# Optimization experiments

Hardware: AMD Instinct MI355X
Metric: run time of the kernel (lower is better)

## Reference

```python
import jax, jax.numpy as jnp
import numpy as np

N_NODES = 100000
N_EDGES = 1600000
IN_F, HID, OUT_F = 50, 256, 121


def setup_inputs() -> dict:
    key = jax.random.key(0)
    ks = jax.random.split(key, 8)
    x = jax.random.normal(ks[0], (N_NODES, IN_F), dtype=jnp.float32)
    edge_index = jax.random.randint(ks[1], (2, N_EDGES), 0, N_NODES, dtype=jnp.int64)
    W1 = jax.random.normal(ks[2], (IN_F, HID), dtype=jnp.float32) * (1.0 / np.sqrt(IN_F))
    b1 = jnp.zeros((HID,), dtype=jnp.float32)
    W2 = jax.random.normal(ks[3], (HID, HID), dtype=jnp.float32) * (1.0 / np.sqrt(HID))
    b2 = jnp.zeros((HID,), dtype=jnp.float32)
    W3 = jax.random.normal(ks[4], (HID, OUT_F), dtype=jnp.float32) * (1.0 / np.sqrt(HID))
    b3 = jnp.zeros((OUT_F,), dtype=jnp.float32)
    return {"x": x, "edge_index": edge_index, "W1": W1, "b1": b1,
            "W2": W2, "b2": b2, "W3": W3, "b3": b3}


def _gcn_norm(edge_index, num_nodes):
    # PyG gcn_norm: add self-loops, symmetric degree normalization.
    loop = jnp.arange(num_nodes, dtype=edge_index.dtype)
    row = jnp.concatenate([edge_index[0], loop])  # source
    col = jnp.concatenate([edge_index[1], loop])  # target (aggregation dim)
    ones = jnp.ones(row.shape[0], dtype=jnp.float32)
    deg = jax.ops.segment_sum(ones, col, num_segments=num_nodes)
    dinv = jnp.where(deg > 0, jax.lax.rsqrt(deg), 0.0)
    norm = dinv[row] * dinv[col]  # [E+N]
    return row, col, norm


def _gcn_conv(x, W, b, row, col, norm, num_nodes):
    h = x @ W                                   # [N, F_out] dense transform
    msg = h[row] * norm[:, None]                # gather + scale  [E+N, F_out]
    agg = jax.ops.segment_sum(msg, col, num_segments=num_nodes)  # scatter-add
    return agg + b


def reference(x, edge_index, W1, b1, W2, b2, W3, b3):
    n = x.shape[0]
    row, col, norm = _gcn_norm(edge_index, n)
    # layer 1 + relu (dropout is identity in eval mode)
    x1 = _gcn_conv(x, W1, b1, row, col, norm, n)
    h = jax.nn.relu(x1)
    # layer 2 + relu
    x1 = _gcn_conv(h, W2, b2, row, col, norm, n)
    h = jax.nn.relu(x1)
    # layer 3; module returns pre-relu output x1 of the last conv
    x1 = _gcn_conv(h, W3, b3, row, col, norm, n)
    return x1
```

## Files before the change

kernel.cpp:

```cpp
#include <hip/hip_runtime.h>


#define IN_F 50
#define HID  256
#define OUT_F 121
#define KP1  64
#define NP3  128
#define MPAD 100096

typedef __attribute__((ext_vector_type(8))) short bf16x8;
typedef __attribute__((ext_vector_type(4))) float f32x4;

__device__ __forceinline__ float bf2f(unsigned short u) {
    union { unsigned int i; float f; } x; x.i = ((unsigned int)u) << 16; return x.f;
}
__device__ __forceinline__ unsigned short f2bf(float f) {
    union { float f; unsigned int i; } x; x.f = f;
    unsigned int r = x.i + 0x7FFFu + ((x.i >> 16) & 1u);
    return (unsigned short)(r >> 16);
}

__device__ __forceinline__ void gl2lds16(const void* g, void* l) {
    __builtin_amdgcn_global_load_lds(
        (const __attribute__((address_space(1))) void*)g,
        (__attribute__((address_space(3))) void*)l, 16, 0, 0);
}

__global__ void k_detect(const int* __restrict__ ei, int* __restrict__ flag, int N) {
    int i = threadIdx.x;
    int lo = ei[2 * i], hi = ei[2 * i + 1];
    int bad = (hi != 0) || ((unsigned)lo >= (unsigned)N);
    unsigned long long m = __ballot(bad);
    if (threadIdx.x == 0) *flag = (m == 0ULL) ? 1 : 0;
}


__global__ void k_count(const int* __restrict__ ei, const int* __restrict__ flag,
                        int* __restrict__ cnt, int E, int N) {
    int t = blockIdx.x * blockDim.x + threadIdx.x;
    if (t >= E) return;
    int f = *flag;
    int c = f ? ei[2 * (E + t)] : ei[E + t];
    c = min(max(c, 0), N - 1);
    atomicAdd(&cnt[c], 1);
}

__global__ __launch_bounds__(1024) void k_scan(const int* __restrict__ cnt,
                                               int* __restrict__ offs,
                                               float* __restrict__ dinv, int n) {
    __shared__ int wsum[16];
    __shared__ int s_carry;
    int lane = threadIdx.x & 63, wid = threadIdx.x >> 6;
    if (threadIdx.x == 0) s_carry = 0;
    __syncthreads();
    for (int base = 0; base < n; base += 4096) {
        int i0 = base + (int)threadIdx.x * 4;
        int v0 = (i0 + 0 < n) ? cnt[i0 + 0] : 0;
        int v1 = (i0 + 1 < n) ? cnt[i0 + 1] : 0;
        int v2 = (i0 + 2 < n) ? cnt[i0 + 2] : 0;
        int v3 = (i0 + 3 < n) ? cnt[i0 + 3] : 0;
        int s1 = v0 + v1, s2 = s1 + v2, tsum = s2 + v3;
        int x = tsum;
        #pragma unroll
        for (int d = 1; d < 64; d <<= 1) {
            int y = __shfl_up(x, d, 64);
            if (lane >= d) x += y;
        }
        if (lane == 63) wsum[wid] = x;
        __syncthreads();
        int wpre = 0;
        #pragma unroll
        for (int j = 0; j < 16; j++) wpre += (j < wid) ? wsum[j] : 0;
        int carry = s_carry;
        int e0 = carry + wpre + x - tsum;
        if (i0 + 0 < n) { offs[i0+0]=e0;    dinv[i0+0]=rsqrtf((float)(v0+1)); }
        if (i0 + 1 < n) { offs[i0+1]=e0+v0; dinv[i0+1]=rsqrtf((float)(v1+1)); }
        if (i0 + 2 < n) { offs[i0+2]=e0+s1; dinv[i0+2]=rsqrtf((float)(v2+1)); }
        if (i0 + 3 < n) { offs[i0+3]=e0+s2; dinv[i0+3]=rsqrtf((float)(v3+1)); }
        __syncthreads();
        if (threadIdx.x == 1023) s_carry = carry + wpre + x;
        __syncthreads();
    }
    if (threadIdx.x == 0) offs[n] = s_carry;
}

__global__ void k_fill8(const int* __restrict__ ei, const int* __restrict__ flag,
                        const int* __restrict__ offs,
                        int* __restrict__ fillc, int* __restrict__ rowidx,
                        int E, int N, int rng) {
    int cell = blockIdx.x & 7;
    int t = (blockIdx.x >> 3) * blockDim.x + threadIdx.x;
    if (t >= E) return;
    int f = *flag;
    int c = f ? ei[2 * (E + t)] : ei[E + t];
    c = min(max(c, 0), N - 1);
    int lo = cell * rng;
    int hi = min(lo + rng, N);
    if (c < lo || c >= hi) return;
    int r = f ? ei[2 * t] : ei[t];
    r = min(max(r, 0), N - 1);
    int pos = offs[c] + atomicAdd(&fillc[c], 1);
    if ((unsigned)pos < (unsigned)E) rowidx[pos] = r;
}

__global__ void k_prep(const float* __restrict__ x, const float* __restrict__ dinv,
                       unsigned short* __restrict__ Xs,
                       const float* __restrict__ W1, unsigned short* __restrict__ Bt1,
                       const float* __restrict__ W2, unsigned short* __restrict__ Bt2,
                       const float* __restrict__ W3, unsigned short* __restrict__ Bt3,
                       int N) {
    int bid = blockIdx.x;
    int npadx = (N * KP1 + 255) / 256;
    if (bid < npadx) {
        int idx = bid * 256 + (int)threadIdx.x;
        if (idx < N * KP1) {
            int node = idx >> 6, k = idx & 63;
            Xs[idx] = (k < IN_F) ? f2bf(dinv[node] * x[node * IN_F + k]) : (unsigned short)0;
        }
        return;
    }
    bid -= npadx;
    if (bid < (HID * KP1) / 256) {
        int idx = bid * 256 + (int)threadIdx.x;
        int nn = idx >> 6, k = idx & 63;
        Bt1[idx] = (k < IN_F) ? f2bf(W1[k * HID + nn]) : (unsigned short)0;
        return;
    }
    bid -= (HID * KP1) / 256;
    if (bid < (HID * HID) / 256) {
        int idx = bid * 256 + (int)threadIdx.x;
        int nn = idx >> 8, k = idx & 255;
        Bt2[idx] = f2bf(W2[k * HID + nn]);
        return;
    }
    bid -= (HID * HID) / 256;
    {
        int idx = bid * 256 + (int)threadIdx.x;
        int nn = idx >> 8, k = idx & 255;
        Bt3[idx] = (nn < OUT_F) ? f2bf(W3[k * OUT_F + nn]) : (unsigned short)0;
    }
}

__global__ __launch_bounds__(256) void k_gemm_lds(const unsigned short* __restrict__ A,
                                                  const unsigned short* __restrict__ Bt,
                                                  const float* __restrict__ dinv,
                                                  const float* __restrict__ bias,
                                                  unsigned short* __restrict__ C,
                                                  int K, int Nout,
                                                  int BIAS, int RELU, int SCALE) {
    __shared__ char lds[16384];
    const int tid = threadIdx.x;
    const int wid = tid >> 6, lane = tid & 63;
    const int wm = wid & 1, wn = wid >> 1;
    const int quad = lane >> 4, ml = lane & 15;
    const int m0 = blockIdx.x * 128;
    const int n0g = blockIdx.y * 128;

    f32x4 acc[4][4];
    #pragma unroll
    for (int a = 0; a < 4; a++)
        #pragma unroll
        for (int b = 0; b < 4; b++) acc[a][b] = (f32x4){0.f, 0.f, 0.f, 0.f};

    for (int kk = 0; kk < K; kk += 32) {
        #pragma unroll
        for (int r = 0; r < 2; r++) {
            int c = r * 256 + tid;
            int row = c >> 2, q = c & 3;
            gl2lds16(A  + (size_t)(m0  + row) * K + kk + q * 8, lds + c * 16);
            gl2lds16(Bt + (size_t)(n0g + row) * K + kk + q * 8, lds + 8192 + c * 16);
        }
        __syncthreads();
        bf16x8 af[4], bfv[4];
        #pragma unroll
        for (int mf = 0; mf < 4; mf++)
            af[mf] = *(const bf16x8*)(lds + ((wm * 64 + mf * 16 + ml) * 64 + quad * 16));
        #pragma unroll
        for (int nf = 0; nf < 4; nf++)
            bfv[nf] = *(const bf16x8*)(lds + 8192 + ((wn * 64 + nf * 16 + ml) * 64 + quad * 16));
        #pragma unroll
        for (int mf = 0; mf < 4; mf++)
            #pragma unroll
            for (int nf = 0; nf < 4; nf++)
                acc[mf][nf] = __builtin_amdgcn_mfma_f32_16x16x32_bf16(af[mf], bfv[nf], acc[mf][nf], 0, 0, 0);
        __syncthreads();
    }

    #pragma unroll
    for (int mf = 0; mf < 4; mf++) {
        int r0 = m0 + wm * 64 + mf * 16 + quad * 4;
        float dd[4] = {1.f, 1.f, 1.f, 1.f};
        if (SCALE) { dd[0]=dinv[r0]; dd[1]=dinv[r0+1]; dd[2]=dinv[r0+2]; dd[3]=dinv[r0+3]; }
        #pragma unroll
        for (int nf = 0; nf < 4; nf++) {
            int col = n0g + wn * 64 + nf * 16 + ml;
            float bb = BIAS ? bias[col] : 0.f;
            #pragma unroll
            for (int i = 0; i < 4; i++) {
                float v = acc[mf][nf][i] + bb;
                if (RELU) v = fmaxf(v, 0.f);
                v *= dd[i];
                C[(size_t)(r0 + i) * Nout + col] = f2bf(v);
            }
        }
    }
}

__global__ __launch_bounds__(256) void k_mlp23(const unsigned short* __restrict__ A,
                                               const unsigned short* __restrict__ B2t,
                                               const unsigned short* __restrict__ B3t,
                                               const float* __restrict__ b2,
                                               const float* __restrict__ dinv,
                                               unsigned short* __restrict__ G) {
    __shared__ char lds[65536];
    const int tid = threadIdx.x;
    const int wid = tid >> 6, lane = tid & 63;
    const int wm = wid & 1, wn = wid >> 1;
    const int quad = lane >> 4, ml = lane & 15;
    const int m0 = blockIdx.x * 128;

    f32x4 acc1[4][8];
    #pragma unroll
    for (int a = 0; a < 4; a++)
        #pragma unroll
        for (int b = 0; b < 8; b++) acc1[a][b] = (f32x4){0.f, 0.f, 0.f, 0.f};

    for (int kk = 0; kk < HID; kk += 32) {
        #pragma unroll
        for (int r = 0; r < 2; r++) {
            int c = r * 256 + tid;
            int row = c >> 2, q = c & 3;
            gl2lds16(A + (size_t)(m0 + row) * HID + kk + q * 8, lds + c * 16);
        }
        #pragma unroll
        for (int r = 0; r < 4; r++) {
            int c = r * 256 + tid;
            int nn = c >> 2, q = c & 3;
            gl2lds16(B2t + (size_t)nn * HID + kk + q * 8, lds + 8192 + c * 16);
        }
        __syncthreads();
        bf16x8 af[4], bv[8];
        #pragma unroll
        for (int mf = 0; mf < 4; mf++)
            af[mf] = *(const bf16x8*)(lds + ((wm * 64 + mf * 16 + ml) * 64 + quad * 16));
        #pragma unroll
        for (int nf = 0; nf < 8; nf++)
            bv[nf] = *(const bf16x8*)(lds + 8192 + ((wn * 128 + nf * 16 + ml) * 64 + quad * 16));
        #pragma unroll
        for (int mf = 0; mf < 4; mf++)
            #pragma unroll
            for (int nf = 0; nf < 8; nf++)
                acc1[mf][nf] = __builtin_amdgcn_mfma_f32_16x16x32_bf16(af[mf], bv[nf], acc1[mf][nf], 0, 0, 0);
        __syncthreads();
    }

    #pragma unroll
    for (int nf = 0; nf < 8; nf++) {
        int col = wn * 128 + nf * 16 + ml;
        float bb = b2[col];
        #pragma unroll
        for (int mf = 0; mf < 4; mf++) {
            int rl = wm * 64 + mf * 16 + quad * 4;
            #pragma unroll
            for (int i = 0; i < 4; i++) {
                int row = rl + i;
                int byte = (row * 512 + col * 2) ^ ((row & 7) << 4);
                *(unsigned short*)(lds + byte) = f2bf(fmaxf(acc1[mf][nf][i] + bb, 0.f));
            }
        }
    }
    __syncthreads();

    f32x4 acc2[4][4];
    #pragma unroll
    for (int a = 0; a < 4; a++)
        #pragma unroll
        for (int b = 0; b < 4; b++) acc2[a][b] = (f32x4){0.f, 0.f, 0.f, 0.f};

    for (int kk = 0; kk < HID; kk += 32) {
        bf16x8 af2[4], bv2[4];
        #pragma unroll
        for (int mf = 0; mf < 4; mf++) {
            int row = wm * 64 + mf * 16 + ml;
            int byte = (row * 512 + kk * 2 + quad * 16) ^ ((row & 7) << 4);
            af2[mf] = *(const bf16x8*)(lds + byte);
        }
        #pragma unroll
        for (int nf = 0; nf < 4; nf++)
            bv2[nf] = *(const bf16x8*)(B3t + (size_t)(wn * 64 + nf * 16 + ml) * HID + kk + quad * 8);
        #pragma unroll
        for (int mf = 0; mf < 4; mf++)
            #pragma unroll
            for (int nf = 0; nf < 4; nf++)
                acc2[mf][nf] = __builtin_amdgcn_mfma_f32_16x16x32_bf16(af2[mf], bv2[nf], acc2[mf][nf], 0, 0, 0);
    }

    #pragma unroll
    for (int mf = 0; mf < 4; mf++) {
        int r0 = m0 + wm * 64 + mf * 16 + quad * 4;
        float dd[4] = {dinv[r0], dinv[r0+1], dinv[r0+2], dinv[r0+3]};
        #pragma unroll
        for (int nf = 0; nf < 4; nf++) {
            int col = wn * 64 + nf * 16 + ml;
            #pragma unroll
            for (int i = 0; i < 4; i++)
                G[(size_t)(r0 + i) * NP3 + col] = f2bf(acc2[mf][nf][i] * dd[i]);
        }
    }
}


__device__ __forceinline__ int rclamp(int r, int N) { return min(max(r, 0), N - 1); }

__global__ void k_aggx(const unsigned short* __restrict__ Xs,
                       const int* __restrict__ offs, const int* __restrict__ rowidx,
                       const float* __restrict__ dinv, unsigned short* __restrict__ Y, int N) {
    int wid = threadIdx.x >> 6, lane = threadIdx.x & 63;
    int sub = lane >> 3, sl = lane & 7;
    int node = blockIdx.x * 32 + wid * 8 + sub;
    int nc = min(node, N - 1);
    int c = sl * 8;
    bf16x8 s = *(const bf16x8*)(Xs + (size_t)nc * KP1 + c);
    float a[8];
    #pragma unroll
    for (int k = 0; k < 8; k++) a[k] = bf2f((unsigned short)s[k]);
    int e = offs[nc], end = offs[nc + 1];
    if (node >= N) { e = 0; end = 0; }
    while (__any(e < end)) {
        int r[4]; float m[4];
        #pragma unroll
        for (int j = 0; j < 4; j++) {
            int idx = e + j;
            m[j] = (idx < end) ? 1.f : 0.f;
            idx = min(idx, end - 1); idx = max(idx, 0);
            r[j] = rclamp(rowidx[idx], N);
        }
        bf16x8 u[4];
        #pragma unroll
        for (int j = 0; j < 4; j++)
            u[j] = *(const bf16x8*)(Xs + (size_t)r[j] * KP1 + c);
        #pragma unroll
        for (int j = 0; j < 4; j++)
            #pragma unroll
            for (int k = 0; k < 8; k++)
                a[k] = fmaf(bf2f((unsigned short)u[j][k]), m[j], a[k]);
        e += 4;
    }
    if (node < N) {
        float dv = dinv[node];
        bf16x8 o;
        #pragma unroll
        for (int k = 0; k < 8; k++) o[k] = (short)f2bf(a[k] * dv);
        *(bf16x8*)(Y + (size_t)node * KP1 + c) = o;
    }
}

__global__ void k_agg256s(const unsigned short* __restrict__ Hn,
                          const int* __restrict__ offs, const int* __restrict__ rowidx,
                          const float* __restrict__ dinv, unsigned short* __restrict__ Y,
                          int N, int half_n) {
    int cell = blockIdx.x & 7;
    int chunk = cell >> 1, half = cell & 1;
    int idx = blockIdx.x >> 3;
    int wid = threadIdx.x >> 6, lane = threadIdx.x & 63;
    int sub = lane >> 3, sl = lane & 7;
    int node = half * half_n + idx * 32 + wid * 8 + sub;
    int hi_end = min((half + 1) * half_n, N);
    int ok = node < hi_end;
    int nc = ok ? node : hi_end - 1;
    int c = chunk * 64 + sl * 8;
    bf16x8 s = *(const bf16x8*)(Hn + (size_t)nc * HID + c);
    float a[8];
    #pragma unroll
    for (int k = 0; k < 8; k++) a[k] = bf2f((unsigned short)s[k]);
    int e = offs[nc], end = offs[nc + 1];
    if (!ok) { e = 0; end = 0; }
    while (__any(e < end)) {
        int r[4]; float m[4];
        #pragma unroll
        for (int j = 0; j < 4; j++) {
            int idx2 = e + j;
            m[j] = (idx2 < end) ? 1.f : 0.f;
            idx2 = min(idx2, end - 1); idx2 = max(idx2, 0);
            r[j] = rclamp(rowidx[idx2], N);
        }
        bf16x8 u[4];
        #pragma unroll
        for (int j = 0; j < 4; j++)
            u[j] = *(const bf16x8*)(Hn + (size_t)r[j] * HID + c);
        #pragma unroll
        for (int j = 0; j < 4; j++)
            #pragma unroll
            for (int k = 0; k < 8; k++)
                a[k] = fmaf(bf2f((unsigned short)u[j][k]), m[j], a[k]);
        e += 4;
    }
    if (ok) {
        float dv = dinv[node];
        bf16x8 o;
        #pragma unroll
        for (int k = 0; k < 8; k++) o[k] = (short)f2bf(a[k] * dv);
        *(bf16x8*)(Y + (size_t)node * HID + c) = o;
    }
}

__global__ void k_aggouts(const unsigned short* __restrict__ G,
                          const int* __restrict__ offs, const int* __restrict__ rowidx,
                          const float* __restrict__ dinv, const float* __restrict__ bias,
                          float* __restrict__ out, int N, int quar_n) {
    int cell = blockIdx.x & 7;
    int chunk = cell >> 2, quar = cell & 3;
    int idx = blockIdx.x >> 3;
    int wid = threadIdx.x >> 6, lane = threadIdx.x & 63;
    int sub = lane >> 3, sl = lane & 7;
    int node = quar * quar_n + idx * 32 + wid * 8 + sub;
    int hi_end = min((quar + 1) * quar_n, N);
    int ok = node < hi_end;
    int nc = ok ? node : hi_end - 1;
    int c = chunk * 64 + sl * 8;
    bf16x8 s = *(const bf16x8*)(G + (size_t)nc * NP3 + c);
    float a[8];
    #pragma unroll
    for (int k = 0; k < 8; k++) a[k] = bf2f((unsigned short)s[k]);
    int e = offs[nc], end = offs[nc + 1];
    if (!ok) { e = 0; end = 0; }
    while (__any(e < end)) {
        int r[4]; float m[4];
        #pragma unroll
        for (int j = 0; j < 4; j++) {
            int idx2 = e + j;
            m[j] = (idx2 < end) ? 1.f : 0.f;
            idx2 = min(idx2, end - 1); idx2 = max(idx2, 0);
            r[j] = rclamp(rowidx[idx2], N);
        }
        bf16x8 u[4];
        #pragma unroll
        for (int j = 0; j < 4; j++)
            u[j] = *(const bf16x8*)(G + (size_t)r[j] * NP3 + c);
        #pragma unroll
        for (int j = 0; j < 4; j++)
            #pragma unroll
            for (int k = 0; k < 8; k++)
                a[k] = fmaf(bf2f((unsigned short)u[j][k]), m[j], a[k]);
        e += 4;
    }
    if (ok) {
        float dv = dinv[node];
        #pragma unroll
        for (int k = 0; k < 8; k++) {
            int col = c + k;
            if (col < OUT_F)
                out[(size_t)node * OUT_F + col] = fmaf(a[k], dv, bias[col]);
        }
    }
}


extern "C" void kernel_launch(void* const* d_in, const int* in_sizes, int n_in,
                              void* d_out, int out_size, void* d_ws, size_t ws_size,
                              hipStream_t stream) {
    const float* x  = (const float*)d_in[0];
    const int*   ei = (const int*)d_in[1];
    const float* W1 = (const float*)d_in[2];
    const float* b1 = (const float*)d_in[3];
    const float* W2 = (const float*)d_in[4];
    const float* b2 = (const float*)d_in[5];
    const float* W3 = (const float*)d_in[6];
    const float* b3 = (const float*)d_in[7];
    float* out = (float*)d_out;

    const int N = in_sizes[0] / IN_F;
    const int E = in_sizes[1] / 2;

    char* w = (char*)d_ws;
    size_t off = 0;
    auto alloc = [&](size_t bytes) -> char* {
        char* p = w + off;
        off += (bytes + 255) & ~(size_t)255;
        return p;
    };
    int*   cnt    = (int*)  alloc((size_t)N * 4);
    int*   fillc  = (int*)  alloc((size_t)N * 4);
    int*   offs   = (int*)  alloc((size_t)(N + 1) * 4);
    float* dinv   = (float*)alloc((size_t)MPAD * 4);
    int*   flag   = (int*)  alloc(256);
    int*   rowidx = (int*)  alloc((size_t)E * 4);
    unsigned short* Bt1 = (unsigned short*)alloc((size_t)HID * KP1 * 2);
    unsigned short* Bt2 = (unsigned short*)alloc((size_t)HID * HID * 2);
    unsigned short* Bt3 = (unsigned short*)alloc((size_t)NP3 * HID * 2);
    unsigned short* bufA = (unsigned short*)alloc((size_t)MPAD * HID * 2);
    unsigned short* bufB = (unsigned short*)alloc((size_t)MPAD * HID * 2);
    unsigned short* Xs  = bufA;
    unsigned short* Y1  = bufB;
    unsigned short* H1s = bufA;
    unsigned short* Y2  = bufB;
    unsigned short* G3  = bufA;

    size_t msz = (size_t)((char*)fillc - (char*)cnt) + (size_t)N * 4;
    hipMemsetAsync(cnt, 0, msz, stream);

    k_detect<<<1, 64, 0, stream>>>(ei, flag, N);
    k_count<<<(E + 255) / 256, 256, 0, stream>>>(ei, flag, cnt, E, N);
    k_scan<<<1, 1024, 0, stream>>>(cnt, offs, dinv, N);
    int rng = (N + 7) / 8;
    k_fill8<<<8 * ((E + 255) / 256), 256, 0, stream>>>(ei, flag, offs, fillc, rowidx, E, N, rng);

    int prep_grid = (N * KP1 + 255) / 256 + (HID * KP1) / 256 + (HID * HID) / 256 + (NP3 * HID) / 256;
    k_prep<<<prep_grid, 256, 0, stream>>>(x, dinv, Xs, W1, Bt1, W2, Bt2, W3, Bt3, N);

    k_aggx<<<(N + 31) / 32, 256, 0, stream>>>(Xs, offs, rowidx, dinv, Y1, N);
    dim3 g1(MPAD / 128, HID / 128);
    k_gemm_lds<<<g1, 256, 0, stream>>>(Y1, Bt1, dinv, b1, H1s, KP1, HID, 1, 1, 1);
    int half_n = (N + 1) / 2;
    int bpc2 = (half_n + 31) / 32;
    k_agg256s<<<8 * bpc2, 256, 0, stream>>>(H1s, offs, rowidx, dinv, Y2, N, half_n);
    k_mlp23<<<MPAD / 128, 256, 0, stream>>>(Y2, Bt2, Bt3, b2, dinv, G3);
    int quar_n = (N + 3) / 4;
    int bpc3 = (quar_n + 31) / 32;
    k_aggouts<<<8 * bpc3, 256, 0, stream>>>(G3, offs, rowidx, dinv, b3, out, N, quar_n);

    (void)n_in; (void)out_size; (void)ws_size;
}
```

Measured before the change: 621.6 us.

## Bucket CSR neighbors by source-range quarter and parallelize the offset scan

Builds the CSR with four sub-buckets per target node, keyed by which quarter of the node range the source falls in. Each node's neighbor list is then ordered by source region, so gathers in the aggregation kernels touch more localized memory. The single-block serial scan becomes a three-kernel multi-block scan, and edge indices are converted once to clamped int32 arrays reused by the count and fill passes. The cost is four times larger count and offset arrays, extra kernel launches, and a split inner loop with more wave-divergent tails per node.

Result: faster. 562.8 us (-9.5%).

```diff
diff --git a/kernel.cpp b/kernel.cpp
--- a/kernel.cpp
+++ b/kernel.cpp
@@ -34,72 +34,110 @@
     if (threadIdx.x == 0) *flag = (m == 0ULL) ? 1 : 0;
 }
 
-
-__global__ void k_count(const int* __restrict__ ei, const int* __restrict__ flag,
-                        int* __restrict__ cnt, int E, int N) {
+__global__ void k_cvt(const int* __restrict__ ei, const int* __restrict__ flag,
+                      int* __restrict__ col32, int* __restrict__ row32, int E, int N) {
     int t = blockIdx.x * blockDim.x + threadIdx.x;
     if (t >= E) return;
     int f = *flag;
     int c = f ? ei[2 * (E + t)] : ei[E + t];
-    c = min(max(c, 0), N - 1);
-    atomicAdd(&cnt[c], 1);
-}
-
-__global__ __launch_bounds__(1024) void k_scan(const int* __restrict__ cnt,
-                                               int* __restrict__ offs,
-                                               float* __restrict__ dinv, int n) {
+    int r = f ? ei[2 * t] : ei[t];
+    col32[t] = min(max(c, 0), N - 1);
+    row32[t] = min(max(r, 0), N - 1);
+}
+
+
+__global__ void k_count4(const int* __restrict__ col32, const int* __restrict__ row32,
+                         int* __restrict__ cnt4, int E, int seglen) {
+    int t = blockIdx.x * blockDim.x + threadIdx.x;
+    if (t >= E) return;
+    int c = col32[t], r = row32[t];
+    atomicAdd(&cnt4[c * 4 + r / seglen], 1);
+}
+
+__global__ __launch_bounds__(1024) void k_scanA(const int* __restrict__ cnt4,
+                                                int* __restrict__ bsum, int n) {
+    __shared__ int ws[16];
+    int tid = threadIdx.x, lane = tid & 63, wid = tid >> 6;
+    int j0 = blockIdx.x * 4096 + tid * 4;
+    int t = 0;
+    #pragma unroll
+    for (int j = 0; j < 4; j++) {
+        int node = j0 + j;
+        if (node < n) { int4 v = *(const int4*)(cnt4 + 4 * node); t += v.x + v.y + v.z + v.w; }
+    }
+    #pragma unroll
+    for (int d = 1; d < 64; d <<= 1) t += __shfl_xor(t, d, 64);
+    if (lane == 0) ws[wid] = t;
+    __syncthreads();
+    if (tid == 0) {
+        int s = 0;
+        #pragma unroll
+        for (int j = 0; j < 16; j++) s += ws[j];
+        bsum[blockIdx.x] = s;
+    }
+}
+
+__global__ void k_scanB(const int* __restrict__ bsum, int* __restrict__ bbase,
+                        int* __restrict__ offs4, int nb, int n4) {
+    int lane = threadIdx.x;
+    int v = (lane < nb) ? bsum[lane] : 0;
+    int x = v;
+    #pragma unroll
+    for (int d = 1; d < 64; d <<= 1) { int y = __shfl_up(x, d, 64); if (lane >= d) x += y; }
+    if (lane < nb) bbase[lane] = x - v;
+    if (lane == nb - 1) offs4[n4] = x;
+}
+
+__global__ __launch_bounds__(1024) void k_scanC(const int* __restrict__ cnt4,
+                                                const int* __restrict__ bbase,
+                                                int* __restrict__ offs4,
+                                                float* __restrict__ dinv, int n) {
     __shared__ int wsum[16];
-    __shared__ int s_carry;
-    int lane = threadIdx.x & 63, wid = threadIdx.x >> 6;
-    if (threadIdx.x == 0) s_carry = 0;
+    int tid = threadIdx.x, lane = tid & 63, wid = tid >> 6;
+    int i0 = blockIdx.x * 4096 + tid * 4;
+    int4 z = {0, 0, 0, 0};
+    int4 c0 = (i0 + 0 < n) ? *(const int4*)(cnt4 + 4 * (i0 + 0)) : z;
+    int4 c1 = (i0 + 1 < n) ? *(const int4*)(cnt4 + 4 * (i0 + 1)) : z;
+    int4 c2 = (i0 + 2 < n) ? *(const int4*)(cnt4 + 4 * (i0 + 2)) : z;
+    int4 c3 = (i0 + 3 < n) ? *(const int4*)(cnt4 + 4 * (i0 + 3)) : z;
+    int v0 = c0.x + c0.y + c0.z + c0.w;
+    int v1 = c1.x + c1.y + c1.z + c1.w;
+    int v2 = c2.x + c2.y + c2.z + c2.w;
+    int v3 = c3.x + c3.y + c3.z + c3.w;
+    int s1 = v0 + v1, s2 = s1 + v2, tsum = s2 + v3;
+    int x = tsum;
+    #pragma unroll
+    for (int d = 1; d < 64; d <<= 1) { int y = __shfl_up(x, d, 64); if (lane >= d) x += y; }
+    if (lane == 63) wsum[wid] = x;
     __syncthreads();
-    for (int base = 0; base < n; base += 4096) {
-        int i0 = base + (int)threadIdx.x * 4;
-        int v0 = (i0 + 0 < n) ? cnt[i0 + 0] : 0;
-        int v1 = (i0 + 1 < n) ? cnt[i0 + 1] : 0;
-        int v2 = (i0 + 2 < n) ? cnt[i0 + 2] : 0;
-        int v3 = (i0 + 3 < n) ? cnt[i0 + 3] : 0;
-        int s1 = v0 + v1, s2 = s1 + v2, tsum = s2 + v3;
-        int x = tsum;
-        #pragma unroll
-        for (int d = 1; d < 64; d <<= 1) {
-            int y = __shfl_up(x, d, 64);
-            if (lane >= d) x += y;
-        }
-        if (lane == 63) wsum[wid] = x;
-        __syncthreads();
-        int wpre = 0;
-        #pragma unroll
-        for (int j = 0; j < 16; j++) wpre += (j < wid) ? wsum[j] : 0;
-        int carry = s_carry;
-        int e0 = carry + wpre + x - tsum;
-        if (i0 + 0 < n) { offs[i0+0]=e0;    dinv[i0+0]=rsqrtf((float)(v0+1)); }
-        if (i0 + 1 < n) { offs[i0+1]=e0+v0; dinv[i0+1]=rsqrtf((float)(v1+1)); }
-        if (i0 + 2 < n) { offs[i0+2]=e0+s1; dinv[i0+2]=rsqrtf((float)(v2+1)); }
-        if (i0 + 3 < n) { offs[i0+3]=e0+s2; dinv[i0+3]=rsqrtf((float)(v3+1)); }
-        __syncthreads();
-        if (threadIdx.x == 1023) s_carry = carry + wpre + x;
-        __syncthreads();
-    }
-    if (threadIdx.x == 0) offs[n] = s_carry;
-}
-
-__global__ void k_fill8(const int* __restrict__ ei, const int* __restrict__ flag,
-                        const int* __restrict__ offs,
-                        int* __restrict__ fillc, int* __restrict__ rowidx,
-                        int E, int N, int rng) {
+    int wpre = 0;
+    #pragma unroll
+    for (int j = 0; j < 16; j++) wpre += (j < wid) ? wsum[j] : 0;
+    int e0 = bbase[blockIdx.x] + wpre + x - tsum;
+    if (i0 + 0 < n) { int4 o; o.x = e0;      o.y = o.x + c0.x; o.z = o.y + c0.y; o.w = o.z + c0.z;
+                      *(int4*)(offs4 + 4 * (i0 + 0)) = o; dinv[i0 + 0] = rsqrtf((float)(v0 + 1)); }
+    if (i0 + 1 < n) { int4 o; o.x = e0 + v0; o.y = o.x + c1.x; o.z = o.y + c1.y; o.w = o.z + c1.z;
+                      *(int4*)(offs4 + 4 * (i0 + 1)) = o; dinv[i0 + 1] = rsqrtf((float)(v1 + 1)); }
+    if (i0 + 2 < n) { int4 o; o.x = e0 + s1; o.y = o.x + c2.x; o.z = o.y + c2.y; o.w = o.z + c2.z;
+                      *(int4*)(offs4 + 4 * (i0 + 2)) = o; dinv[i0 + 2] = rsqrtf((float)(v2 + 1)); }
+    if (i0 + 3 < n) { int4 o; o.x = e0 + s2; o.y = o.x + c3.x; o.z = o.y + c3.y; o.w = o.z + c3.z;
+                      *(int4*)(offs4 + 4 * (i0 + 3)) = o; dinv[i0 + 3] = rsqrtf((float)(v3 + 1)); }
+}
+
+__global__ void k_fill8(const int* __restrict__ col32, const int* __restrict__ row32,
+                        const int* __restrict__ offs4,
+                        int* __restrict__ fillc4, int* __restrict__ rowidx,
+                        int E, int N, int rng, int seglen) {
     int cell = blockIdx.x & 7;
     int t = (blockIdx.x >> 3) * blockDim.x + threadIdx.x;
     if (t >= E) return;
-    int f = *flag;
-    int c = f ? ei[2 * (E + t)] : ei[E + t];
-    c = min(max(c, 0), N - 1);
+    int c = col32[t];
     int lo = cell * rng;
     int hi = min(lo + rng, N);
     if (c < lo || c >= hi) return;
-    int r = f ? ei[2 * t] : ei[t];
-    r = min(max(r, 0), N - 1);
-    int pos = offs[c] + atomicAdd(&fillc[c], 1);
+    int r = row32[t];
+    int key = c * 4 + r / seglen;
+    int pos = offs4[key] + atomicAdd(&fillc4[key], 1);
     if ((unsigned)pos < (unsigned)E) rowidx[pos] = r;
 }
 
@@ -310,10 +348,8 @@
 }
 
 
-__device__ __forceinline__ int rclamp(int r, int N) { return min(max(r, 0), N - 1); }
-
 __global__ void k_aggx(const unsigned short* __restrict__ Xs,
-                       const int* __restrict__ offs, const int* __restrict__ rowidx,
+                       const int* __restrict__ offs4, const int* __restrict__ rowidx,
                        const float* __restrict__ dinv, unsigned short* __restrict__ Y, int N) {
     int wid = threadIdx.x >> 6, lane = threadIdx.x & 63;
     int sub = lane >> 3, sl = lane & 7;
@@ -324,27 +360,34 @@
     float a[8];
     #pragma unroll
     for (int k = 0; k < 8; k++) a[k] = bf2f((unsigned short)s[k]);
-    int e = offs[nc], end = offs[nc + 1];
-    if (node >= N) { e = 0; end = 0; }
-    while (__any(e < end)) {
-        int r[4]; float m[4];
-        #pragma unroll
-        for (int j = 0; j < 4; j++) {
-            int idx = e + j;
-            m[j] = (idx < end) ? 1.f : 0.f;
-            idx = min(idx, end - 1); idx = max(idx, 0);
-            r[j] = rclamp(rowidx[idx], N);
-        }
-        bf16x8 u[4];
-        #pragma unroll
-        for (int j = 0; j < 4; j++)
-            u[j] = *(const bf16x8*)(Xs + (size_t)r[j] * KP1 + c);
-        #pragma unroll
-        for (int j = 0; j < 4; j++)
-            #pragma unroll
-            for (int k = 0; k < 8; k++)
-                a[k] = fmaf(bf2f((unsigned short)u[j][k]), m[j], a[k]);
-        e += 4;
+    int4 ob = *(const int4*)(offs4 + 4 * nc);
+    int oe = offs4[4 * nc + 4];
+    int st[5] = {ob.x, ob.y, ob.z, ob.w, oe};
+    int live = node < N;
+    #pragma unroll
+    for (int sg = 0; sg < 4; sg++) {
+        int e = st[sg], end = st[sg + 1];
+        if (!live) { e = 0; end = 0; }
+        while (__any(e < end)) {
+            int r[4]; float m[4];
+            #pragma unroll
+            for (int j = 0; j < 4; j++) {
+                int idx = e + j;
+                m[j] = (idx < end) ? 1.f : 0.f;
+                idx = min(idx, end - 1); idx = max(idx, 0);
+                r[j] = rowidx[idx];
+            }
+            bf16x8 u[4];
+            #pragma unroll
+            for (int j = 0; j < 4; j++)
+                u[j] = *(const bf16x8*)(Xs + (size_t)r[j] * KP1 + c);
+            #pragma unroll
+            for (int j = 0; j < 4; j++)
+                #pragma unroll
+                for (int k = 0; k < 8; k++)
+                    a[k] = fmaf(bf2f((unsigned short)u[j][k]), m[j], a[k]);
+            e += 4;
+        }
     }
     if (node < N) {
         float dv = dinv[node];
@@ -356,7 +399,7 @@
 }
 
 __global__ void k_agg256s(const unsigned short* __restrict__ Hn,
-                          const int* __restrict__ offs, const int* __restrict__ rowidx,
+                          const int* __restrict__ offs4, const int* __restrict__ rowidx,
                           const float* __restrict__ dinv, unsigned short* __restrict__ Y,
                           int N, int half_n) {
     int cell = blockIdx.x & 7;
@@ -373,27 +416,33 @@
     float a[8];
     #pragma unroll
     for (int k = 0; k < 8; k++) a[k] = bf2f((unsigned short)s[k]);
-    int e = offs[nc], end = offs[nc + 1];
-    if (!ok) { e = 0; end = 0; }
-    while (__any(e < end)) {
-        int r[4]; float m[4];
-        #pragma unroll
-        for (int j = 0; j < 4; j++) {
-            int idx2 = e + j;
-            m[j] = (idx2 < end) ? 1.f : 0.f;
-            idx2 = min(idx2, end - 1); idx2 = max(idx2, 0);
-            r[j] = rclamp(rowidx[idx2], N);
-        }
-        bf16x8 u[4];
-        #pragma unroll
-        for (int j = 0; j < 4; j++)
-            u[j] = *(const bf16x8*)(Hn + (size_t)r[j] * HID + c);
-        #pragma unroll
-        for (int j = 0; j < 4; j++)
-            #pragma unroll
-            for (int k = 0; k < 8; k++)
-                a[k] = fmaf(bf2f((unsigned short)u[j][k]), m[j], a[k]);
-        e += 4;
+    int4 ob = *(const int4*)(offs4 + 4 * nc);
+    int oe = offs4[4 * nc + 4];
+    int st[5] = {ob.x, ob.y, ob.z, ob.w, oe};
+    #pragma unroll
+    for (int sg = 0; sg < 4; sg++) {
+        int e = st[sg], end = st[sg + 1];
+        if (!ok) { e = 0; end = 0; }
+        while (__any(e < end)) {
+            int r[4]; float m[4];
+            #pragma unroll
+            for (int j = 0; j < 4; j++) {
+                int idx2 = e + j;
+                m[j] = (idx2 < end) ? 1.f : 0.f;
+                idx2 = min(idx2, end - 1); idx2 = max(idx2, 0);
+                r[j] = rowidx[idx2];
+            }
+            bf16x8 u[4];
+            #pragma unroll
+            for (int j = 0; j < 4; j++)
+                u[j] = *(const bf16x8*)(Hn + (size_t)r[j] * HID + c);
+            #pragma unroll
+            for (int j = 0; j < 4; j++)
+                #pragma unroll
+                for (int k = 0; k < 8; k++)
+                    a[k] = fmaf(bf2f((unsigned short)u[j][k]), m[j], a[k]);
+            e += 4;
+        }
     }
     if (ok) {
         float dv = dinv[node];
@@ -405,7 +454,7 @@
 }
 
 __global__ void k_aggouts(const unsigned short* __restrict__ G,
-                          const int* __restrict__ offs, const int* __restrict__ rowidx,
+                          const int* __restrict__ offs4, const int* __restrict__ rowidx,
                           const float* __restrict__ dinv, const float* __restrict__ bias,
                           float* __restrict__ out, int N, int quar_n) {
     int cell = blockIdx.x & 7;
@@ -422,7 +471,7 @@
     float a[8];
     #pragma unroll
     for (int k = 0; k < 8; k++) a[k] = bf2f((unsigned short)s[k]);
-    int e = offs[nc], end = offs[nc + 1];
+    int e = offs4[4 * nc], end = offs4[4 * nc + 4];
     if (!ok) { e = 0; end = 0; }
     while (__any(e < end)) {
         int r[4]; float m[4];
@@ -431,7 +480,7 @@
             int idx2 = e + j;
             m[j] = (idx2 < end) ? 1.f : 0.f;
             idx2 = min(idx2, end - 1); idx2 = max(idx2, 0);
-            r[j] = rclamp(rowidx[idx2], N);
+            r[j] = rowidx[idx2];
         }
         bf16x8 u[4];
         #pragma unroll
@@ -479,11 +528,15 @@
         off += (bytes + 255) & ~(size_t)255;
         return p;
     };
-    int*   cnt    = (int*)  alloc((size_t)N * 4);
-    int*   fillc  = (int*)  alloc((size_t)N * 4);
-    int*   offs   = (int*)  alloc((size_t)(N + 1) * 4);
+    int*   cnt4   = (int*)  alloc((size_t)N * 16);
+    int*   fillc4 = (int*)  alloc((size_t)N * 16);
+    int*   offs4  = (int*)  alloc((size_t)(4 * N + 1) * 4);
     float* dinv   = (float*)alloc((size_t)MPAD * 4);
     int*   flag   = (int*)  alloc(256);
+    int*   bsum   = (int*)  alloc(256);
+    int*   bbase  = (int*)  alloc(256);
+    int*   col32  = (int*)  alloc((size_t)E * 4);
+    int*   row32  = (int*)  alloc((size_t)E * 4);
     int*   rowidx = (int*)  alloc((size_t)E * 4);
     unsigned short* Bt1 = (unsigned short*)alloc((size_t)HID * KP1 * 2);
     unsigned short* Bt2 = (unsigned short*)alloc((size_t)HID * HID * 2);
@@ -496,28 +549,34 @@
     unsigned short* Y2  = bufB;
     unsigned short* G3  = bufA;
 
-    size_t msz = (size_t)((char*)fillc - (char*)cnt) + (size_t)N * 4;
-    hipMemsetAsync(cnt, 0, msz, stream);
+    size_t msz = (size_t)((char*)fillc4 - (char*)cnt4) + (size_t)N * 16;
+    hipMemsetAsync(cnt4, 0, msz, stream);
+
+    const int seglen = (N + 3) / 4;
+    const int nsc = (N + 4095) / 4096;
 
     k_detect<<<1, 64, 0, stream>>>(ei, flag, N);
-    k_count<<<(E + 255) / 256, 256, 0, stream>>>(ei, flag, cnt, E, N);
-    k_scan<<<1, 1024, 0, stream>>>(cnt, offs, dinv, N);
+    k_cvt<<<(E + 255) / 256, 256, 0, stream>>>(ei, flag, col32, row32, E, N);
+    k_count4<<<(E + 255) / 256, 256, 0, stream>>>(col32, row32, cnt4, E, seglen);
+    k_scanA<<<nsc, 1024, 0, stream>>>(cnt4, bsum, N);
+    k_scanB<<<1, 64, 0, stream>>>(bsum, bbase, offs4, nsc, 4 * N);
+    k_scanC<<<nsc, 1024, 0, stream>>>(cnt4, bbase, offs4, dinv, N);
     int rng = (N + 7) / 8;
-    k_fill8<<<8 * ((E + 255) / 256), 256, 0, stream>>>(ei, flag, offs, fillc, rowidx, E, N, rng);
+    k_fill8<<<8 * ((E + 255) / 256), 256, 0, stream>>>(col32, row32, offs4, fillc4, rowidx, E, N, rng, seglen);
 
     int prep_grid = (N * KP1 + 255) / 256 + (HID * KP1) / 256 + (HID * HID) / 256 + (NP3 * HID) / 256;
     k_prep<<<prep_grid, 256, 0, stream>>>(x, dinv, Xs, W1, Bt1, W2, Bt2, W3, Bt3, N);
 
-    k_aggx<<<(N + 31) / 32, 256, 0, stream>>>(Xs, offs, rowidx, dinv, Y1, N);
+    k_aggx<<<(N + 31) / 32, 256, 0, stream>>>(Xs, offs4, rowidx, dinv, Y1, N);
     dim3 g1(MPAD / 128, HID / 128);
     k_gemm_lds<<<g1, 256, 0, stream>>>(Y1, Bt1, dinv, b1, H1s, KP1, HID, 1, 1, 1);
     int half_n = (N + 1) / 2;
     int bpc2 = (half_n + 31) / 32;
-    k_agg256s<<<8 * bpc2, 256, 0, stream>>>(H1s, offs, rowidx, dinv, Y2, N, half_n);
+    k_agg256s<<<8 * bpc2, 256, 0, stream>>>(H1s, offs4, rowidx, dinv, Y2, N, half_n);
     k_mlp23<<<MPAD / 128, 256, 0, stream>>>(Y2, Bt2, Bt3, b2, dinv, G3);
     int quar_n = (N + 3) / 4;
     int bpc3 = (quar_n + 31) / 32;
-    k_aggouts<<<8 * bpc3, 256, 0, stream>>>(G3, offs, rowidx, dinv, b3, out, N, quar_n);
+    k_aggouts<<<8 * bpc3, 256, 0, stream>>>(G3, offs4, rowidx, dinv, b3, out, N, quar_n);
 
     (void)n_in; (void)out_size; (void)ws_size;
 }
```
